# Optimization experiments

Hardware: AMD Instinct MI355X
Metric: run time of the kernel (lower is better)

The kernel has to match this reference:

```python
import jax, jax.numpy as jnp
import numpy as np

D_MODEL = 1024
HEADS = 16
D_HEAD = D_MODEL // HEADS


def setup_inputs() -> dict:
    key = jax.random.key(0)
    ks = jax.random.split(key, 7)
    s = 1.0 / np.sqrt(D_MODEL)
    x = jax.random.normal(ks[0], (4, 2048, D_MODEL), dtype=jnp.float32)
    Wq = jax.random.uniform(ks[1], (D_MODEL, D_MODEL), jnp.float32, -s, s)
    bq = jax.random.uniform(ks[2], (D_MODEL,), jnp.float32, -s, s)
    Wk = jax.random.uniform(ks[3], (D_MODEL, D_MODEL), jnp.float32, -s, s)
    bk = jax.random.uniform(ks[4], (D_MODEL,), jnp.float32, -s, s)
    Wv = jax.random.uniform(ks[5], (D_MODEL, D_MODEL), jnp.float32, -s, s)
    bv = jax.random.uniform(ks[6], (D_MODEL,), jnp.float32, -s, s)
    return {"x": x, "Wq": Wq, "bq": bq, "Wk": Wk, "bk": bk, "Wv": Wv, "bv": bv}


def reference(x, Wq, bq, Wk, bk, Wv, bv):
    B, S, D = x.shape
    # QKV projections, split heads: [B, H, S, Dh]
    def split(t):
        return t.reshape(B, S, HEADS, D_HEAD).transpose(0, 2, 1, 3)
    q = split(x @ Wq + bq)
    k = split(x @ Wk + bk)
    v = split(x @ Wv + bv)
    scores = jnp.einsum('bhqd,bhkd->bhqk', q, k) / np.sqrt(D_HEAD).astype(jnp.float32)
    attn = jax.nn.softmax(scores, axis=-1)
    out = jnp.einsum('bhqk,bhkd->bhqd', attn, v)
    return out.transpose(0, 2, 1, 3).reshape(B, S, D)
```

## Files before the change

### kernel.cpp

```cpp
#include <hip/hip_runtime.h>

typedef _Float16 f16;
typedef __attribute__((ext_vector_type(2))) _Float16 f16x2;
typedef __attribute__((ext_vector_type(2))) __fp16   hf16x2;
typedef __attribute__((ext_vector_type(4))) _Float16 f16x4;
typedef __attribute__((ext_vector_type(8))) _Float16 f16x8;
typedef __attribute__((ext_vector_type(4))) float    f32x4;

#define D_MODEL 1024
#define HEADS   16
#define DH      64
#define SEQ     2048
#define BATCH   4
#define SSCALE  0.1803368801111204f

__device__ __forceinline__ void gload_lds16(const void* g, void* lds) {
  __builtin_amdgcn_global_load_lds(
      (const __attribute__((address_space(1))) unsigned int*)g,
      (__attribute__((address_space(3))) unsigned int*)lds, 16, 0, 0);
}

__global__ __launch_bounds__(256) void prep_kernel(const float* __restrict__ x,
                                                   const float* __restrict__ Wq,
                                                   const float* __restrict__ Wk,
                                                   const float* __restrict__ Wv,
                                                   f16* __restrict__ xb,
                                                   f16* __restrict__ wt) {
  if (blockIdx.x < 8192) {
    int i = blockIdx.x * 256 + threadIdx.x;
    float4 v = ((const float4*)x)[i];
    f16x4 h;
    h[0] = (f16)v.x; h[1] = (f16)v.y; h[2] = (f16)v.z; h[3] = (f16)v.w;
    ((f16x4*)xb)[i] = h;
    return;
  }
  int bid = blockIdx.x - 8192;
  int z = bid >> 8, rem = bid & 255;
  const float* W = z == 0 ? Wq : (z == 1 ? Wk : Wv);
  f16* out = wt + (size_t)z * D_MODEL * D_MODEL;
  __shared__ float tile[64][65];
  int n0 = (rem & 15) * 64, k0 = (rem >> 4) * 64;
  int tx = threadIdx.x & 63, ty = threadIdx.x >> 6;
#pragma unroll
  for (int r = 0; r < 16; ++r)
    tile[ty * 16 + r][tx] = W[(size_t)(k0 + ty * 16 + r) * D_MODEL + n0 + tx];
  __syncthreads();
#pragma unroll
  for (int r = 0; r < 16; ++r)
    out[(size_t)(n0 + ty * 16 + r) * D_MODEL + k0 + tx] = (f16)tile[tx][ty * 16 + r];
}

__global__ __launch_bounds__(256, 3) void qkv_gemm_kernel(
    const f16* __restrict__ xb, const f16* __restrict__ wt_all,
    const float* __restrict__ bq, const float* __restrict__ bk, const float* __restrict__ bv,
    f16* __restrict__ qout, f16* __restrict__ kout, f16* __restrict__ vtout) {
  const int z = blockIdx.z;
  const f16* wt = wt_all + (size_t)z * D_MODEL * D_MODEL;
  const float* bias = z == 0 ? bq : (z == 1 ? bk : bv);
  const int n0 = blockIdx.x * 128, m0 = blockIdx.y * 128;

  __shared__ f16 As[2][128 * 32];
  __shared__ f16 Bs[2][128 * 32];

  const int tid = threadIdx.x;
  const int lane = tid & 63, w = tid >> 6;
  const int quad = lane >> 4, l15 = lane & 15;
  const int wm = w & 1, wn = w >> 1;

  const int pce = (quad ^ ((l15 >> 1) & 3)) * 8;
  const int aoff = wm * 2048 + l15 * 32 + pce;
  const int boff = wn * 2048 + l15 * 32 + pce;

  int srow[2], scl[2];
#pragma unroll
  for (int c = 0; c < 2; ++c) {
    int slot = (w * 2 + c) * 64 + lane;
    srow[c] = slot >> 2;
    scl[c] = (slot & 3) ^ ((srow[c] >> 1) & 3);
  }

  f32x4 acc[4][4];
#pragma unroll
  for (int i = 0; i < 4; ++i)
#pragma unroll
    for (int j = 0; j < 4; ++j) acc[i][j] = (f32x4){0.f, 0.f, 0.f, 0.f};

#pragma unroll
  for (int c = 0; c < 2; ++c) {
    gload_lds16(xb + (size_t)(m0 + srow[c]) * D_MODEL + scl[c] * 8, &As[0][(w * 2 + c) * 512]);
    gload_lds16(wt + (size_t)(n0 + srow[c]) * D_MODEL + scl[c] * 8, &Bs[0][(w * 2 + c) * 512]);
  }

  f16x8 aP[4], bP[4];
  for (int it = 0; it < 32; ++it) {
    const int buf = it & 1;
    __syncthreads();
    if (it < 31) {
      const int kn = (it + 1) * 32;
#pragma unroll
      for (int c = 0; c < 2; ++c) {
        gload_lds16(xb + (size_t)(m0 + srow[c]) * D_MODEL + kn + scl[c] * 8, &As[buf ^ 1][(w * 2 + c) * 512]);
        gload_lds16(wt + (size_t)(n0 + srow[c]) * D_MODEL + kn + scl[c] * 8, &Bs[buf ^ 1][(w * 2 + c) * 512]);
      }
    }
    f16x8 aC[4], bC[4];
#pragma unroll
    for (int mt = 0; mt < 4; ++mt) aC[mt] = *(const f16x8*)(&As[buf][aoff + mt * 512]);
#pragma unroll
    for (int nt = 0; nt < 4; ++nt) bC[nt] = *(const f16x8*)(&Bs[buf][boff + nt * 512]);
    if (it) {
#pragma unroll
      for (int mt = 0; mt < 4; ++mt)
#pragma unroll
        for (int nt = 0; nt < 4; ++nt)
          acc[mt][nt] = __builtin_amdgcn_mfma_f32_16x16x32_f16(aP[mt], bP[nt], acc[mt][nt], 0, 0, 0);
    }
#pragma unroll
    for (int t = 0; t < 4; ++t) { aP[t] = aC[t]; bP[t] = bC[t]; }
  }
#pragma unroll
  for (int mt = 0; mt < 4; ++mt)
#pragma unroll
    for (int nt = 0; nt < 4; ++nt)
      acc[mt][nt] = __builtin_amdgcn_mfma_f32_16x16x32_f16(aP[mt], bP[nt], acc[mt][nt], 0, 0, 0);

  const float sc = (z == 0) ? SSCALE : 1.0f;
  float bcol[4];
#pragma unroll
  for (int nt = 0; nt < 4; ++nt) bcol[nt] = bias[n0 + wn * 64 + nt * 16 + l15];

  if (z < 2) {
    f16* out = (z == 0) ? qout : kout;
#pragma unroll
    for (int mt = 0; mt < 4; ++mt) {
      int mbase = m0 + wm * 64 + mt * 16 + quad * 4;
#pragma unroll
      for (int nt = 0; nt < 4; ++nt) {
        int n = n0 + wn * 64 + nt * 16 + l15;
        int h = n >> 6, dh = n & 63;
#pragma unroll
        for (int r = 0; r < 4; ++r) {
          int m = mbase + r;
          int b = m >> 11, s = m & 2047;
          out[((size_t)(b * HEADS + h) * SEQ + s) * DH + dh] = (f16)((acc[mt][nt][r] + bcol[nt]) * sc);
        }
      }
    }
  } else {
#pragma unroll
    for (int mt = 0; mt < 4; ++mt) {
      int mbase = m0 + wm * 64 + mt * 16 + quad * 4;
      int b = mbase >> 11, s = mbase & 2047;
#pragma unroll
      for (int nt = 0; nt < 4; ++nt) {
        int n = n0 + wn * 64 + nt * 16 + l15;
        int h = n >> 6, dh = n & 63;
        f16x4 v;
#pragma unroll
        for (int r = 0; r < 4; ++r) v[r] = (f16)(acc[mt][nt][r] + bcol[nt]);
        *(f16x4*)(vtout + ((size_t)(b * HEADS + h) * DH + dh) * SEQ + s) = v;
      }
    }
  }
}

__global__ __launch_bounds__(256, 4) void attn_kernel(
    const f16* __restrict__ q, const f16* __restrict__ k, const f16* __restrict__ vt,
    float* __restrict__ out) {
  const int bh = blockIdx.x;
  const int s0 = blockIdx.y * 128;
  const int b = bh >> 4, h = bh & 15;
  const int tid = threadIdx.x, lane = tid & 63, w = tid >> 6;
  const int quad = lane >> 4, l15 = lane & 15;
  const int qh = quad >> 1, q1 = quad & 1;

  __shared__ f16 Ks[2][64 * 64];
  __shared__ f16 Vs[3][64 * 64];

  const f16* qbase = q + ((size_t)bh * SEQ + s0 + w * 32) * DH;
  const f16* kbase = k + (size_t)bh * SEQ * DH;
  const f16* vbase = vt + (size_t)bh * DH * SEQ;

  f16x8 qf[2][2];
#pragma unroll
  for (int qt = 0; qt < 2; ++qt)
#pragma unroll
    for (int ks = 0; ks < 2; ++ks)
      qf[qt][ks] = *(const f16x8*)(qbase + (qt * 16 + l15) * DH + ks * 32 + quad * 8);

  int koff[2];
  koff[0] = l15 * 64 + ((quad ^ (l15 & 7)) * 8);
  koff[1] = l15 * 64 + (((4 + quad) ^ (l15 & 7)) * 8);
  int voff[4];
#pragma unroll
  for (int ks = 0; ks < 4; ++ks)
    voff[ks] = l15 * 64 + (((ks * 2 + qh) ^ (l15 & 7)) * 8) + q1 * 4;

  int srow[2], scl[2];
#pragma unroll
  for (int c = 0; c < 2; ++c) {
    int slot = (w * 2 + c) * 64 + lane;
    srow[c] = slot >> 3;
    scl[c] = (slot & 7) ^ (srow[c] & 7);
  }

  float lsum[2] = {0.f, 0.f};
  f32x4 o[4][2];
#pragma unroll
  for (int i = 0; i < 4; ++i)
#pragma unroll
    for (int j = 0; j < 2; ++j) o[i][j] = (f32x4){0.f, 0.f, 0.f, 0.f};
  const f32x4 Zero = (f32x4){0.f, 0.f, 0.f, 0.f};

#pragma unroll
  for (int c = 0; c < 2; ++c) {
    gload_lds16(kbase + (size_t)srow[c] * DH + scl[c] * 8, &Ks[0][(w * 2 + c) * 512]);
    gload_lds16(vbase + (size_t)srow[c] * SEQ + scl[c] * 8, &Vs[0][(w * 2 + c) * 512]);
  }

  f16x4 pbP[4][2];
  int vb = 0, vbn = 1, vbp = 2;

  for (int kt = 0; kt < SEQ / 64; ++kt) {
    const int kb = kt & 1;
    __syncthreads();
    if (kt < SEQ / 64 - 1) {
      const int kn = (kt + 1) * 64;
#pragma unroll
      for (int c = 0; c < 2; ++c) {
        gload_lds16(kbase + (size_t)(kn + srow[c]) * DH + scl[c] * 8, &Ks[kb ^ 1][(w * 2 + c) * 512]);
        gload_lds16(vbase + (size_t)srow[c] * SEQ + kn + scl[c] * 8, &Vs[vbn][(w * 2 + c) * 512]);
      }
    }

    f32x4 st[4][2];
#pragma unroll
    for (int mt = 0; mt < 4; ++mt) {
      f16x8 af0 = *(const f16x8*)(&Ks[kb][koff[0] + mt * 1024]);
      f16x8 af1 = *(const f16x8*)(&Ks[kb][koff[1] + mt * 1024]);
#pragma unroll
      for (int qt = 0; qt < 2; ++qt) {
        st[mt][qt] = __builtin_amdgcn_mfma_f32_16x16x32_f16(af0, qf[qt][0], Zero, 0, 0, 0);
        st[mt][qt] = __builtin_amdgcn_mfma_f32_16x16x32_f16(af1, qf[qt][1], st[mt][qt], 0, 0, 0);
      }
    }

    if (kt) {
#pragma unroll
      for (int ks = 0; ks < 4; ++ks)
#pragma unroll
        for (int mt = 0; mt < 4; ++mt) {
          f16x4 va = *(const f16x4*)(&Vs[vbp][voff[ks] + mt * 1024]);
#pragma unroll
          for (int qt = 0; qt < 2; ++qt)
            o[mt][qt] = __builtin_amdgcn_mfma_f32_16x16x16f16(va, pbP[ks][qt], o[mt][qt], 0, 0, 0);
        }
    }

#pragma unroll
    for (int ks = 0; ks < 4; ++ks)
#pragma unroll
      for (int qt = 0; qt < 2; ++qt) {
        float e0 = __builtin_amdgcn_exp2f(st[ks][qt][0]);
        float e1 = __builtin_amdgcn_exp2f(st[ks][qt][1]);
        float e2 = __builtin_amdgcn_exp2f(st[ks][qt][2]);
        float e3 = __builtin_amdgcn_exp2f(st[ks][qt][3]);
        lsum[qt] += (e0 + e1) + (e2 + e3);
        f16x2 p01 = __builtin_bit_cast(f16x2, __builtin_amdgcn_cvt_pkrtz(e0, e1));
        f16x2 p23 = __builtin_bit_cast(f16x2, __builtin_amdgcn_cvt_pkrtz(e2, e3));
        pbP[ks][qt] = __builtin_shufflevector(p01, p23, 0, 1, 2, 3);
      }

    int t = vbp; vbp = vb; vb = vbn; vbn = t;
  }

#pragma unroll
  for (int ks = 0; ks < 4; ++ks)
#pragma unroll
    for (int mt = 0; mt < 4; ++mt) {
      f16x4 va = *(const f16x4*)(&Vs[vbp][voff[ks] + mt * 1024]);
#pragma unroll
      for (int qt = 0; qt < 2; ++qt)
        o[mt][qt] = __builtin_amdgcn_mfma_f32_16x16x16f16(va, pbP[ks][qt], o[mt][qt], 0, 0, 0);
    }

#pragma unroll
  for (int qt = 0; qt < 2; ++qt) {
    float l = lsum[qt];
    l += __shfl_xor(l, 16, 64);
    l += __shfl_xor(l, 32, 64);
    float inv = 1.f / l;
    int sq = s0 + w * 32 + qt * 16 + l15;
    float* obase = out + ((size_t)b * SEQ + sq) * D_MODEL + h * DH;
#pragma unroll
    for (int mt = 0; mt < 4; ++mt) {
      f32x4 vv;
#pragma unroll
      for (int r = 0; r < 4; ++r) vv[r] = o[mt][qt][r] * inv;
      *(f32x4*)(obase + mt * 16 + quad * 4) = vv;
    }
  }
}

extern "C" void kernel_launch(void* const* d_in, const int* in_sizes, int n_in,
                              void* d_out, int out_size, void* d_ws, size_t ws_size,
                              hipStream_t stream) {
  const float* x  = (const float*)d_in[0];
  const float* Wq = (const float*)d_in[1];
  const float* bq = (const float*)d_in[2];
  const float* Wk = (const float*)d_in[3];
  const float* bk = (const float*)d_in[4];
  const float* Wv = (const float*)d_in[5];
  const float* bv = (const float*)d_in[6];
  float* out = (float*)d_out;

  char* ws = (char*)d_ws;
  f16* xb = (f16*)ws;
  f16* wt = (f16*)(ws + (size_t)16 * 1024 * 1024);
  f16* q  = (f16*)(ws + (size_t)22 * 1024 * 1024);
  f16* kk = q + (size_t)BATCH * SEQ * D_MODEL;
  f16* vt = kk + (size_t)BATCH * SEQ * D_MODEL;

  prep_kernel<<<8192 + 768, 256, 0, stream>>>(x, Wq, Wk, Wv, xb, wt);
  qkv_gemm_kernel<<<dim3(8, 64, 3), 256, 0, stream>>>(xb, wt, bq, bk, bv, q, kk, vt);
  attn_kernel<<<dim3(64, 16), 256, 0, stream>>>(q, kk, vt, out);
}
```

Measured before the change: 283.1 us.

## Pre-tile V into swizzled 64x64 blocks and drop software-pipelined PV stage

The projection kernel now writes V^T in a per-key-tile blocked, pre-swizzled layout, so each 64x64 tile is contiguous and can be copied to LDS with linear 16-byte loads. The attention kernel reads V as 128-bit LDS loads split into two MFMA operands, which halves the V LDS read instructions. The V buffer count drops from three to two, and the one-iteration-delayed P·V schedule is removed in favour of computing P·V in the same iteration. This reduces LDS use and address arithmetic, but it gives up overlap between the exp work and the PV MFMAs of the previous tile.

```diff
diff --git a/kernel.cpp b/kernel.cpp
--- a/kernel.cpp
+++ b/kernel.cpp
@@ -150,7 +150,8 @@
 #pragma unroll
     for (int mt = 0; mt < 4; ++mt) {
       int mbase = m0 + wm * 64 + mt * 16 + quad * 4;
-      int b = mbase >> 11, s = mbase & 2047;
+      int b = mbase >> 11, seq = mbase & 2047;
+      int kt = seq >> 6;
 #pragma unroll
       for (int nt = 0; nt < 4; ++nt) {
         int n = n0 + wn * 64 + nt * 16 + l15;
@@ -158,7 +159,9 @@
         f16x4 v;
 #pragma unroll
         for (int r = 0; r < 4; ++r) v[r] = (f16)(acc[mt][nt][r] + bcol[nt]);
-        *(f16x4*)(vtout + ((size_t)(b * HEADS + h) * DH + dh) * SEQ + s) = v;
+        int phys = (quad * 2 + (mt >> 1)) ^ (dh & 7);
+        size_t off = (((size_t)(b * HEADS + h) * 32 + kt) * 4096) + dh * 64 + phys * 8 + (mt & 1) * 4;
+        *(f16x4*)(vtout + off) = v;
       }
     }
   }
@@ -172,10 +175,9 @@
   const int b = bh >> 4, h = bh & 15;
   const int tid = threadIdx.x, lane = tid & 63, w = tid >> 6;
   const int quad = lane >> 4, l15 = lane & 15;
-  const int qh = quad >> 1, q1 = quad & 1;
 
   __shared__ f16 Ks[2][64 * 64];
-  __shared__ f16 Vs[3][64 * 64];
+  __shared__ f16 Vs[2][64 * 64];
 
   const f16* qbase = q + ((size_t)bh * SEQ + s0 + w * 32) * DH;
   const f16* kbase = k + (size_t)bh * SEQ * DH;
@@ -191,10 +193,9 @@
   int koff[2];
   koff[0] = l15 * 64 + ((quad ^ (l15 & 7)) * 8);
   koff[1] = l15 * 64 + (((4 + quad) ^ (l15 & 7)) * 8);
-  int voff[4];
-#pragma unroll
-  for (int ks = 0; ks < 4; ++ks)
-    voff[ks] = l15 * 64 + (((ks * 2 + qh) ^ (l15 & 7)) * 8) + q1 * 4;
+  int voff2[2];
+  voff2[0] = l15 * 64 + (((quad * 2) ^ (l15 & 7)) * 8);
+  voff2[1] = l15 * 64 + (((quad * 2 + 1) ^ (l15 & 7)) * 8);
 
   int srow[2], scl[2];
 #pragma unroll
@@ -203,6 +204,8 @@
     srow[c] = slot >> 3;
     scl[c] = (slot & 7) ^ (srow[c] & 7);
   }
+  const int vslot = ((w * 2) * 64 + lane) * 8;
+  const int vslot2 = ((w * 2 + 1) * 64 + lane) * 8;
 
   float lsum[2] = {0.f, 0.f};
   f32x4 o[4][2];
@@ -213,31 +216,28 @@
   const f32x4 Zero = (f32x4){0.f, 0.f, 0.f, 0.f};
 
 #pragma unroll
-  for (int c = 0; c < 2; ++c) {
+  for (int c = 0; c < 2; ++c)
     gload_lds16(kbase + (size_t)srow[c] * DH + scl[c] * 8, &Ks[0][(w * 2 + c) * 512]);
-    gload_lds16(vbase + (size_t)srow[c] * SEQ + scl[c] * 8, &Vs[0][(w * 2 + c) * 512]);
-  }
-
-  f16x4 pbP[4][2];
-  int vb = 0, vbn = 1, vbp = 2;
+  gload_lds16(vbase + vslot,  &Vs[0][(w * 2) * 512]);
+  gload_lds16(vbase + vslot2, &Vs[0][(w * 2 + 1) * 512]);
 
   for (int kt = 0; kt < SEQ / 64; ++kt) {
-    const int kb = kt & 1;
+    const int buf = kt & 1;
     __syncthreads();
     if (kt < SEQ / 64 - 1) {
       const int kn = (kt + 1) * 64;
 #pragma unroll
-      for (int c = 0; c < 2; ++c) {
-        gload_lds16(kbase + (size_t)(kn + srow[c]) * DH + scl[c] * 8, &Ks[kb ^ 1][(w * 2 + c) * 512]);
-        gload_lds16(vbase + (size_t)srow[c] * SEQ + kn + scl[c] * 8, &Vs[vbn][(w * 2 + c) * 512]);
-      }
+      for (int c = 0; c < 2; ++c)
+        gload_lds16(kbase + (size_t)(kn + srow[c]) * DH + scl[c] * 8, &Ks[buf ^ 1][(w * 2 + c) * 512]);
+      gload_lds16(vbase + (kt + 1) * 4096 + vslot,  &Vs[buf ^ 1][(w * 2) * 512]);
+      gload_lds16(vbase + (kt + 1) * 4096 + vslot2, &Vs[buf ^ 1][(w * 2 + 1) * 512]);
     }
 
     f32x4 st[4][2];
 #pragma unroll
     for (int mt = 0; mt < 4; ++mt) {
-      f16x8 af0 = *(const f16x8*)(&Ks[kb][koff[0] + mt * 1024]);
-      f16x8 af1 = *(const f16x8*)(&Ks[kb][koff[1] + mt * 1024]);
+      f16x8 af0 = *(const f16x8*)(&Ks[buf][koff[0] + mt * 1024]);
+      f16x8 af1 = *(const f16x8*)(&Ks[buf][koff[1] + mt * 1024]);
 #pragma unroll
       for (int qt = 0; qt < 2; ++qt) {
         st[mt][qt] = __builtin_amdgcn_mfma_f32_16x16x32_f16(af0, qf[qt][0], Zero, 0, 0, 0);
@@ -245,18 +245,7 @@
       }
     }
 
-    if (kt) {
-#pragma unroll
-      for (int ks = 0; ks < 4; ++ks)
-#pragma unroll
-        for (int mt = 0; mt < 4; ++mt) {
-          f16x4 va = *(const f16x4*)(&Vs[vbp][voff[ks] + mt * 1024]);
-#pragma unroll
-          for (int qt = 0; qt < 2; ++qt)
-            o[mt][qt] = __builtin_amdgcn_mfma_f32_16x16x16f16(va, pbP[ks][qt], o[mt][qt], 0, 0, 0);
-        }
-    }
-
+    f16x4 pb[4][2];
 #pragma unroll
     for (int ks = 0; ks < 4; ++ks)
 #pragma unroll
@@ -268,21 +257,23 @@
         lsum[qt] += (e0 + e1) + (e2 + e3);
         f16x2 p01 = __builtin_bit_cast(f16x2, __builtin_amdgcn_cvt_pkrtz(e0, e1));
         f16x2 p23 = __builtin_bit_cast(f16x2, __builtin_amdgcn_cvt_pkrtz(e2, e3));
-        pbP[ks][qt] = __builtin_shufflevector(p01, p23, 0, 1, 2, 3);
-      }
-
-    int t = vbp; vbp = vb; vb = vbn; vbn = t;
-  }
-
-#pragma unroll
-  for (int ks = 0; ks < 4; ++ks)
-#pragma unroll
-    for (int mt = 0; mt < 4; ++mt) {
-      f16x4 va = *(const f16x4*)(&Vs[vbp][voff[ks] + mt * 1024]);
-#pragma unroll
-      for (int qt = 0; qt < 2; ++qt)
-        o[mt][qt] = __builtin_amdgcn_mfma_f32_16x16x16f16(va, pbP[ks][qt], o[mt][qt], 0, 0, 0);
-    }
+        pb[ks][qt] = __builtin_shufflevector(p01, p23, 0, 1, 2, 3);
+      }
+
+#pragma unroll
+    for (int half = 0; half < 2; ++half)
+#pragma unroll
+      for (int mt = 0; mt < 4; ++mt) {
+        f16x8 v8 = *(const f16x8*)(&Vs[buf][voff2[half] + mt * 1024]);
+        f16x4 vaA = __builtin_shufflevector(v8, v8, 0, 1, 2, 3);
+        f16x4 vaB = __builtin_shufflevector(v8, v8, 4, 5, 6, 7);
+#pragma unroll
+        for (int qt = 0; qt < 2; ++qt) {
+          o[mt][qt] = __builtin_amdgcn_mfma_f32_16x16x16f16(vaA, pb[half * 2][qt], o[mt][qt], 0, 0, 0);
+          o[mt][qt] = __builtin_amdgcn_mfma_f32_16x16x16f16(vaB, pb[half * 2 + 1][qt], o[mt][qt], 0, 0, 0);
+        }
+      }
+  }
 
 #pragma unroll
   for (int qt = 0; qt < 2; ++qt) {
```

After: 256.0 us. 1.11x faster.
